# Performance work log

Measured on AMD Instinct MI355X. Metric: run time of the kernel, lower is better.

Reference implementation:

```python
import jax, jax.numpy as jnp
import numpy as np

B, S, E, H, W = 1, 4096, 1024, 16, 256
D = E // H
SCALE = D ** -0.5


def setup_inputs() -> dict:
    key = jax.random.key(0)
    k1, k2, k3 = jax.random.split(key, 3)
    x = jax.random.normal(k1, (B, S, E), dtype=jnp.float32)
    # torch Linear weight is [out,in]; we store transposed [in,out] so y = x @ w
    w_qkv = jax.random.normal(k2, (E, 3 * E), dtype=jnp.float32) * (E ** -0.5)
    w_out = jax.random.normal(k3, (E, E), dtype=jnp.float32) * (E ** -0.5)
    # sliding-window causal mask: key j allowed for query i iff i-W < j <= i
    q_idx = jnp.arange(S)[:, None]
    k_idx = jnp.arange(S)[None, :]
    allowed_mask = (k_idx <= q_idx) & (k_idx > q_idx - W)  # [S,S] bool
    allowed_mask = allowed_mask[None, None]  # [1,1,S,S]
    return {"x": x, "allowed_mask": allowed_mask, "w_qkv": w_qkv, "w_out": w_out}


def reference(x, allowed_mask, w_qkv, w_out):
    b, s, e = x.shape
    qkv = (x @ w_qkv).reshape(b, s, 3, H, D)
    q, k, v = jnp.moveaxis(qkv, 2, 0)  # each [b,s,H,D]
    q = q.transpose(0, 2, 1, 3)  # [b,H,s,D]
    k = k.transpose(0, 2, 1, 3)
    v = v.transpose(0, 2, 1, 3)
    scores = jnp.einsum('bhsd,bhtd->bhst', q, k) * SCALE  # [b,H,s,s]
    scores = jnp.where(allowed_mask, scores, -jnp.inf)
    attn = jax.nn.softmax(scores, axis=-1)
    out = jnp.einsum('bhst,bhtd->bhsd', attn, v)  # [b,H,s,D]
    out = out.transpose(0, 2, 1, 3).reshape(b, s, e)
    return out @ w_out
```

## Files before the change

### kernel.cpp

```cpp
#include <hip/hip_runtime.h>
#include <hip/hip_bf16.h>

#define S_LEN 4096
#define EMB   1024
#define NH    16
#define HD    64
#define WIN   256
#define SCALE 0.125f

typedef __attribute__((ext_vector_type(8))) short short8;
typedef __attribute__((ext_vector_type(4))) float f32x4;
typedef __attribute__((ext_vector_type(4))) unsigned short us4;

__device__ inline unsigned short f2b(float x) {
    __hip_bfloat16 b = __float2bfloat16(x);
    return *reinterpret_cast<unsigned short*>(&b);
}

__device__ inline void gld_lds16(const unsigned short* g, unsigned short* l) {
    __builtin_amdgcn_global_load_lds(
        (const __attribute__((address_space(1))) unsigned int*)g,
        (__attribute__((address_space(3))) unsigned int*)l,
        16, 0, 0);
}

__global__ __launch_bounds__(256) void cast_f32_bf16(const float* __restrict__ in,
                                                     unsigned short* __restrict__ out,
                                                     int n) {
    int i = blockIdx.x * blockDim.x + threadIdx.x;
    int stride = gridDim.x * blockDim.x;
    for (; i < n; i += stride) out[i] = f2b(in[i]);
}

__global__ __launch_bounds__(256) void transpose_cast(const float* __restrict__ in,
                                                      unsigned short* __restrict__ out,
                                                      int R, int C) {
    __shared__ alignas(16) unsigned short t[64 * 72];
    const int tid = threadIdx.x;
    const int r0 = blockIdx.y * 64, c0 = blockIdx.x * 64;

    const int rr = tid >> 4, cc = (tid & 15) * 4;
    #pragma unroll
    for (int i = 0; i < 4; ++i) {
        float4 v = *reinterpret_cast<const float4*>(&in[(size_t)(r0 + rr + i * 16) * C + c0 + cc]);
        t[(cc + 0) * 72 + rr + i * 16] = f2b(v.x);
        t[(cc + 1) * 72 + rr + i * 16] = f2b(v.y);
        t[(cc + 2) * 72 + rr + i * 16] = f2b(v.z);
        t[(cc + 3) * 72 + rr + i * 16] = f2b(v.w);
    }
    __syncthreads();

    const int wr = tid >> 2, wk = (tid & 3) * 16;
    #pragma unroll
    for (int p = 0; p < 2; ++p)
        *reinterpret_cast<uint4*>(&out[(size_t)(c0 + wr) * R + r0 + wk + p * 8]) =
            *reinterpret_cast<const uint4*>(&t[wr * 72 + wk + p * 8]);
}

template <int MODE>
__global__ __launch_bounds__(256) void gemm_bt(const unsigned short* __restrict__ A,
                                               const unsigned short* __restrict__ Bt,
                                               void* __restrict__ Cout,
                                               unsigned short* __restrict__ vT,
                                               int M, int N, int K) {
    __shared__ alignas(16) unsigned short smem[17408];
    unsigned short* As = smem;
    unsigned short* Bs = smem + 4096;

    const int tid  = threadIdx.x;
    const int lane = tid & 63;
    const int w    = tid >> 6;
    const int quad = lane >> 4;
    const int l16  = lane & 15;

    const int m0 = blockIdx.y * 128;
    const int n0 = blockIdx.x * 128;
    const int m_off = (w & 1) * 64;
    const int n_off = (w >> 1) * 64;

    const int srow = tid >> 2;
    const int skof = (tid & 3) * 8;

    f32x4 acc[4][4];
    #pragma unroll
    for (int i = 0; i < 4; ++i)
        #pragma unroll
        for (int j = 0; j < 4; ++j)
            acc[i][j] = (f32x4){0.f, 0.f, 0.f, 0.f};

    for (int bk = 0; bk < K; bk += 32) {
        __syncthreads();
        #pragma unroll
        for (int inst = 0; inst < 2; ++inst) {
            gld_lds16(A  + (size_t)(m0 + inst * 64 + srow) * K + bk + skof,
                      As + inst * 2048 + w * 512);
            gld_lds16(Bt + (size_t)(n0 + inst * 64 + srow) * K + bk + skof,
                      Bs + inst * 2048 + w * 512);
        }
        __syncthreads();

        short8 af[4], bf[4];
        #pragma unroll
        for (int i = 0; i < 4; ++i)
            af[i] = *reinterpret_cast<const short8*>(&As[(m_off + i * 16 + l16) * 32 + quad * 8]);
        #pragma unroll
        for (int j = 0; j < 4; ++j)
            bf[j] = *reinterpret_cast<const short8*>(&Bs[(n_off + j * 16 + l16) * 32 + quad * 8]);

        #pragma unroll
        for (int i = 0; i < 4; ++i)
            #pragma unroll
            for (int j = 0; j < 4; ++j)
                acc[i][j] = __builtin_amdgcn_mfma_f32_16x16x32_bf16(
                    af[i], bf[j], acc[i][j], 0, 0, 0);
    }

    if (MODE == 0) {
        float* C = (float*)Cout;
        #pragma unroll
        for (int i = 0; i < 4; ++i)
            #pragma unroll
            for (int r = 0; r < 4; ++r) {
                const size_t row = m0 + m_off + i * 16 + quad * 4 + r;
                #pragma unroll
                for (int j = 0; j < 4; ++j)
                    C[row * N + n0 + n_off + j * 16 + l16] = acc[i][j][r];
            }
    } else if (n0 < 2048) {
        unsigned short* C = (unsigned short*)Cout;
        #pragma unroll
        for (int i = 0; i < 4; ++i)
            #pragma unroll
            for (int r = 0; r < 4; ++r) {
                const size_t row = m0 + m_off + i * 16 + quad * 4 + r;
                #pragma unroll
                for (int j = 0; j < 4; ++j)
                    C[row * N + n0 + n_off + j * 16 + l16] = f2b(acc[i][j][r]);
            }
    } else {
        __syncthreads();
        #pragma unroll
        for (int i = 0; i < 4; ++i) {
            const int ss = m_off + i * 16 + quad * 4;
            #pragma unroll
            for (int j = 0; j < 4; ++j) {
                const int dd = n_off + j * 16 + l16;
                us4 pk = {f2b(acc[i][j][0]), f2b(acc[i][j][1]),
                          f2b(acc[i][j][2]), f2b(acc[i][j][3])};
                *reinterpret_cast<us4*>(&smem[dd * 136 + ss]) = pk;
            }
        }
        __syncthreads();
        #pragma unroll
        for (int p = 0; p < 8; ++p) {
            const int t  = p * 256 + tid;
            const int dd = t >> 4;
            const int sc = (t & 15) * 8;
            *reinterpret_cast<uint4*>(&vT[(size_t)(n0 - 2048 + dd) * S_LEN + m0 + sc]) =
                *reinterpret_cast<const uint4*>(&smem[dd * 136 + sc]);
        }
    }
}

__global__ __launch_bounds__(256) void attn_mfma(const unsigned short* __restrict__ qkv,
                                                 const unsigned short* __restrict__ vT,
                                                 const unsigned short* __restrict__ zbuf,
                                                 unsigned short* __restrict__ outb) {
    __shared__ alignas(16) unsigned short lds[40960];
    unsigned short* KtP = lds;
    unsigned short* Vt  = lds + 20480;

    const int raw  = blockIdx.x + (blockIdx.y << 6);
    const int xcd  = raw & 7;
    const int slot = raw >> 3;
    const int q0   = (xcd * 8 + (slot & 7)) * 64;
    const int h    = slot >> 3;

    const int tid  = threadIdx.x;
    const int w    = tid >> 6;
    const int lane = tid & 63;
    const int quad = lane >> 4;
    const int l16  = lane & 15;
    const int kbase = q0 - 256;

    #pragma unroll
    for (int i = 0; i < 10; ++i) {
        const int fc  = i * 256 + tid;
        const int row = fc >> 3, p = fc & 7;
        const int c   = p ^ (row & 7);
        const int j   = kbase + row;
        const unsigned short* src = (j >= 0)
            ? qkv + (size_t)j * 3072 + EMB + h * 64 + c * 8 : zbuf;
        gld_lds16(src, KtP + (i * 256 + w * 64) * 8);
    }
    #pragma unroll
    for (int i = 0; i < 10; ++i) {
        const int fc = i * 256 + tid;
        const int d  = fc / 40, pp = fc % 40;
        const int cc = (pp & ~7) | ((pp & 7) ^ (d & 7));
        const int j0 = kbase + cc * 8;
        const unsigned short* src = (j0 >= 0)
            ? vT + (size_t)(h * 64 + d) * S_LEN + kbase + cc * 8 : zbuf;
        gld_lds16(src, Vt + (i * 256 + w * 64) * 8);
    }
    const unsigned short* qrow = qkv + (size_t)(q0 + w * 16 + l16) * 3072 + h * 64;
    short8 aq[2];
    aq[0] = *reinterpret_cast<const short8*>(qrow + quad * 8);
    aq[1] = *reinterpret_cast<const short8*>(qrow + 32 + quad * 8);

    __syncthreads();

    f32x4 accs[20];
    #pragma unroll
    for (int nb = 0; nb < 20; ++nb) accs[nb] = (f32x4){0.f, 0.f, 0.f, 0.f};

    #pragma unroll
    for (int ks = 0; ks < 2; ++ks)
        #pragma unroll
        for (int nb = 0; nb < 20; ++nb) {
            const int row = nb * 16 + l16;
            const int p   = (ks * 4 + quad) ^ (row & 7);
            const short8 bfr = *reinterpret_cast<const short8*>(&KtP[row * 64 + p * 8]);
            accs[nb] = __builtin_amdgcn_mfma_f32_16x16x32_bf16(aq[ks], bfr, accs[nb], 0, 0, 0);
        }

    __syncthreads();

    const int i0 = q0 + w * 16 + quad * 4;
    float rmax[4] = {-1e30f, -1e30f, -1e30f, -1e30f};
    #pragma unroll
    for (int nb = 0; nb < 20; ++nb) {
        const int j = kbase + nb * 16 + l16;
        #pragma unroll
        for (int r = 0; r < 4; ++r) {
            const int i = i0 + r;
            const bool ok = (j >= 0) & (j <= i) & (j > i - WIN);
            const float s = accs[nb][r] * SCALE;
            if (ok) rmax[r] = fmaxf(rmax[r], s);
        }
    }
    #pragma unroll
    for (int r = 0; r < 4; ++r)
        #pragma unroll
        for (int off = 1; off < 16; off <<= 1)
            rmax[r] = fmaxf(rmax[r], __shfl_xor(rmax[r], off, 64));

    float rsum[4] = {0.f, 0.f, 0.f, 0.f};
    #pragma unroll
    for (int nb = 0; nb < 20; ++nb) {
        const int j = kbase + nb * 16 + l16;
        const int col = nb * 16 + l16;
        const int cch = col >> 3, e = col & 7;
        #pragma unroll
        for (int r = 0; r < 4; ++r) {
            const int i = i0 + r;
            const bool ok = (j >= 0) & (j <= i) & (j > i - WIN);
            const float ev = ok ? __expf(accs[nb][r] * SCALE - rmax[r]) : 0.f;
            rsum[r] += ev;
            const int rw  = w * 16 + quad * 4 + r;
            const int pos = (cch & ~7) | ((cch & 7) ^ (rw & 7));
            KtP[rw * 320 + pos * 8 + e] = f2b(ev);
        }
    }
    float inv[4];
    #pragma unroll
    for (int r = 0; r < 4; ++r) {
        #pragma unroll
        for (int off = 1; off < 16; off <<= 1)
            rsum[r] += __shfl_xor(rsum[r], off, 64);
        inv[r] = 1.f / rsum[r];
    }

    f32x4 acco[4];
    #pragma unroll
    for (int nb2 = 0; nb2 < 4; ++nb2) acco[nb2] = (f32x4){0.f, 0.f, 0.f, 0.f};

    #pragma unroll
    for (int ks = 0; ks < 10; ++ks) {
        const int prow = w * 16 + l16;
        const int cc   = ks * 4 + quad;
        const int ppos = (cc & ~7) | ((cc & 7) ^ (prow & 7));
        const short8 af = *reinterpret_cast<const short8*>(&KtP[prow * 320 + ppos * 8]);
        #pragma unroll
        for (int nb2 = 0; nb2 < 4; ++nb2) {
            const int d    = nb2 * 16 + l16;
            const int vpos = (cc & ~7) | ((cc & 7) ^ (d & 7));
            const short8 bfr = *reinterpret_cast<const short8*>(&Vt[d * 320 + vpos * 8]);
            acco[nb2] = __builtin_amdgcn_mfma_f32_16x16x32_bf16(af, bfr, acco[nb2], 0, 0, 0);
        }
    }

    #pragma unroll
    for (int nb2 = 0; nb2 < 4; ++nb2)
        #pragma unroll
        for (int r = 0; r < 4; ++r)
            outb[(size_t)(q0 + w * 16 + quad * 4 + r) * EMB + h * 64 + nb2 * 16 + l16] =
                f2b(acco[nb2][r] * inv[r]);
}

extern "C" void kernel_launch(void* const* d_in, const int* in_sizes, int n_in,
                              void* d_out, int out_size, void* d_ws, size_t ws_size,
                              hipStream_t stream) {
    const float* x     = (const float*)d_in[0];
    const float* w_qkv = (const float*)d_in[2];
    const float* w_out = (const float*)d_in[3];
    float* out = (float*)d_out;

    char* ws = (char*)d_ws;
    unsigned short* xb     = (unsigned short*)(ws);
    unsigned short* wqkvT  = (unsigned short*)(ws + (8u  << 20));
    unsigned short* woutT  = (unsigned short*)(ws + (14u << 20));
    unsigned short* qkvb   = (unsigned short*)(ws + (16u << 20));
    unsigned short* attnb  = (unsigned short*)(ws + (48u << 20));
    unsigned short* vT     = (unsigned short*)(ws + (56u << 20));
    unsigned short* zbuf   = (unsigned short*)(ws + (64u << 20));

    hipMemsetAsync(zbuf, 0, 4096, stream);

    cast_f32_bf16<<<4096, 256, 0, stream>>>(x, xb, S_LEN * EMB);
    transpose_cast<<<dim3(48, 16), 256, 0, stream>>>(w_qkv, wqkvT, EMB, 3 * EMB);
    transpose_cast<<<dim3(16, 16), 256, 0, stream>>>(w_out, woutT, EMB, EMB);

    gemm_bt<1><<<dim3(3 * EMB / 128, S_LEN / 128), 256, 0, stream>>>(
        xb, wqkvT, qkvb, vT, S_LEN, 3 * EMB, EMB);

    attn_mfma<<<dim3(S_LEN / 64, NH), 256, 0, stream>>>(qkvb, vT, zbuf, attnb);

    gemm_bt<0><<<dim3(EMB / 128, S_LEN / 128), 256, 0, stream>>>(
        attnb, woutT, out, nullptr, S_LEN, EMB, EMB);
}
```

Measured before the change: 209.3 us.

## Double GEMM K-tile to 64 with XOR-swizzled LDS layout

The bf16 GEMM now stages a 64-wide K slice per iteration instead of 32. This halves the number of barrier pairs and global-to-LDS load rounds per output tile. The LDS layout uses an XOR swizzle on 16-byte chunks by row, intended to avoid bank conflicts on the 128-byte row stride during MFMA fragment reads. LDS use per block rises to 32 KB, which may reduce occupancy.

```diff
diff --git a/kernel.cpp b/kernel.cpp
--- a/kernel.cpp
+++ b/kernel.cpp
@@ -65,7 +65,7 @@
                                                int M, int N, int K) {
     __shared__ alignas(16) unsigned short smem[17408];
     unsigned short* As = smem;
-    unsigned short* Bs = smem + 4096;
+    unsigned short* Bs = smem + 8192;
 
     const int tid  = threadIdx.x;
     const int lane = tid & 63;
@@ -78,8 +78,8 @@
     const int m_off = (w & 1) * 64;
     const int n_off = (w >> 1) * 64;
 
-    const int srow = tid >> 2;
-    const int skof = (tid & 3) * 8;
+    const int s_row = tid >> 3;
+    const int s_c0  = tid & 7;
 
     f32x4 acc[4][4];
     #pragma unroll
@@ -88,31 +88,41 @@
         for (int j = 0; j < 4; ++j)
             acc[i][j] = (f32x4){0.f, 0.f, 0.f, 0.f};
 
-    for (int bk = 0; bk < K; bk += 32) {
+    for (int bk = 0; bk < K; bk += 64) {
         __syncthreads();
         #pragma unroll
-        for (int inst = 0; inst < 2; ++inst) {
-            gld_lds16(A  + (size_t)(m0 + inst * 64 + srow) * K + bk + skof,
-                      As + inst * 2048 + w * 512);
-            gld_lds16(Bt + (size_t)(n0 + inst * 64 + srow) * K + bk + skof,
-                      Bs + inst * 2048 + w * 512);
+        for (int p = 0; p < 4; ++p) {
+            const int row = p * 32 + s_row;
+            const int c   = s_c0 ^ (row & 7);
+            gld_lds16(A  + (size_t)(m0 + row) * K + bk + c * 8,
+                      As + (p * 256 + w * 64) * 8);
+            gld_lds16(Bt + (size_t)(n0 + row) * K + bk + c * 8,
+                      Bs + (p * 256 + w * 64) * 8);
         }
         __syncthreads();
 
-        short8 af[4], bf[4];
-        #pragma unroll
-        for (int i = 0; i < 4; ++i)
-            af[i] = *reinterpret_cast<const short8*>(&As[(m_off + i * 16 + l16) * 32 + quad * 8]);
-        #pragma unroll
-        for (int j = 0; j < 4; ++j)
-            bf[j] = *reinterpret_cast<const short8*>(&Bs[(n_off + j * 16 + l16) * 32 + quad * 8]);
-
-        #pragma unroll
-        for (int i = 0; i < 4; ++i)
-            #pragma unroll
-            for (int j = 0; j < 4; ++j)
-                acc[i][j] = __builtin_amdgcn_mfma_f32_16x16x32_bf16(
-                    af[i], bf[j], acc[i][j], 0, 0, 0);
+        #pragma unroll
+        for (int ks = 0; ks < 2; ++ks) {
+            short8 af[4], bf[4];
+            #pragma unroll
+            for (int i = 0; i < 4; ++i) {
+                const int r = m_off + i * 16 + l16;
+                af[i] = *reinterpret_cast<const short8*>(
+                    &As[r * 64 + ((ks * 4 + quad) ^ (r & 7)) * 8]);
+            }
+            #pragma unroll
+            for (int j = 0; j < 4; ++j) {
+                const int r = n_off + j * 16 + l16;
+                bf[j] = *reinterpret_cast<const short8*>(
+                    &Bs[r * 64 + ((ks * 4 + quad) ^ (r & 7)) * 8]);
+            }
+            #pragma unroll
+            for (int i = 0; i < 4; ++i)
+                #pragma unroll
+                for (int j = 0; j < 4; ++j)
+                    acc[i][j] = __builtin_amdgcn_mfma_f32_16x16x32_bf16(
+                        af[i], bf[j], acc[i][j], 0, 0, 0);
+        }
     }
 
     if (MODE == 0) {
```

Result: faster. 200.3 us (-4.3%).
